# Kernel tuning notes

Hardware: AMD Instinct MI355X
Metric: run time of the kernel (lower is better)

Reference implementation:

```python
import jax, jax.numpy as jnp
import numpy as np

D_MODEL = 2048
NUM_HEADS = 16
D_K = D_MODEL // NUM_HEADS


def setup_inputs() -> dict:
    key = jax.random.key(0)
    ks = jax.random.split(key, 7)
    B, S = 4, 2048
    scale = 1.0 / np.sqrt(D_MODEL)
    return {
        "q": jax.random.normal(ks[0], (B, S, D_MODEL), dtype=jnp.float32),
        "k": jax.random.normal(ks[1], (B, S, D_MODEL), dtype=jnp.float32),
        "v": jax.random.normal(ks[2], (B, S, D_MODEL), dtype=jnp.float32),
        "w_q": jax.random.normal(ks[3], (D_MODEL, D_MODEL), dtype=jnp.float32) * scale,
        "w_k": jax.random.normal(ks[4], (D_MODEL, D_MODEL), dtype=jnp.float32) * scale,
        "w_v": jax.random.normal(ks[5], (D_MODEL, D_MODEL), dtype=jnp.float32) * scale,
        "w_o": jax.random.normal(ks[6], (D_MODEL, D_MODEL), dtype=jnp.float32) * scale,
    }


def reference(q, k, v, w_q, w_k, w_v, w_o):
    B, S, _ = q.shape
    # torch Linear (bias=False): y = x @ W.T
    def proj_heads(x, w):
        y = jnp.einsum("bsd,ed->bse", x, w)  # [B,S,D]
        return y.reshape(B, S, NUM_HEADS, D_K).transpose(0, 2, 1, 3)  # [B,H,S,Dk]

    qh = proj_heads(q, w_q)
    kh = proj_heads(k, w_k)
    vh = proj_heads(v, w_v)

    # scaled dot-product attention (padding_mask=None, dropout inactive in eval)
    logits = jnp.einsum("bhqd,bhkd->bhqk", qh, kh) / jnp.sqrt(jnp.float32(D_K))
    probs = jax.nn.softmax(logits, axis=-1)
    attn = jnp.einsum("bhqk,bhkd->bhqd", probs, vh)  # [B,H,S,Dk]

    attn = attn.transpose(0, 2, 1, 3).reshape(B, S, NUM_HEADS * D_K)
    return jnp.einsum("bsd,ed->bse", attn, w_o)
```

## Files before the change

kernel.cpp:

```cpp
#include <hip/hip_runtime.h>
#include <hip/hip_bf16.h>
#include <cstdio>

using bf16 = __hip_bfloat16;
typedef __attribute__((ext_vector_type(8))) __bf16 bf16x8;
typedef __attribute__((ext_vector_type(4))) float f32x4;

#define DI static __device__ __forceinline__

DI f32x4 mfma16(bf16x8 a, bf16x8 b, f32x4 c) {
  return __builtin_amdgcn_mfma_f32_16x16x32_bf16(a, b, c, 0, 0, 0);
}

DI void gload16(const bf16* g, bf16* lds_base) {
  __builtin_amdgcn_global_load_lds(
      (const __attribute__((address_space(1))) unsigned int*)g,
      (__attribute__((address_space(3))) unsigned int*)lds_base,
      16, 0, 0);
}

DI bf16x8 ld8(const bf16* p) { return *(const bf16x8*)p; }

DI unsigned pack_bf16(float lo, float hi) {
  bf16 l = __float2bfloat16(lo), h = __float2bfloat16(hi);
  unsigned short ul = *(unsigned short*)&l, uh = *(unsigned short*)&h;
  return ((unsigned)uh << 16) | (unsigned)ul;
}

__global__ __launch_bounds__(256) void cast_bf16_kernel(const float* __restrict__ in,
                                                        bf16* __restrict__ out, int n4) {
  int i = blockIdx.x * 256 + threadIdx.x;
  if (i >= n4) return;
  float4 v = reinterpret_cast<const float4*>(in)[i];
  bf16 o4[4] = {__float2bfloat16(v.x), __float2bfloat16(v.y),
                __float2bfloat16(v.z), __float2bfloat16(v.w)};
  reinterpret_cast<ushort4*>(out)[i] = *reinterpret_cast<ushort4*>(o4);
}

template<int OUT_F32>
__global__ __launch_bounds__(256) void gemm_bt(const bf16* __restrict__ A,
                                               const bf16* __restrict__ B,
                                               void* __restrict__ Cout,
                                               int M, int N, int K) {
  __shared__ bf16 As[128 * 64];
  __shared__ bf16 Bs[128 * 64];
  const int lane = threadIdx.x & 63;
  const int wave = threadIdx.x >> 6;
  const int wm = wave >> 1, wn = wave & 1;
  const int nwg = gridDim.x * gridDim.y;
  const int cpx = nwg >> 3;
  int id = blockIdx.x + gridDim.x * blockIdx.y;
  id = (id & 7) * cpx + (id >> 3);
  const int row0 = (id / gridDim.x) * 128;
  const int col0 = (id % gridDim.x) * 128;
  const int l4 = lane >> 4, l15 = lane & 15;
  const int lr = lane >> 3, lc = lane & 7;

  f32x4 acc[4][4] = {};

  for (int k0 = 0; k0 < K; k0 += 64) {
#pragma unroll
    for (int i = 0; i < 4; ++i) {
      const int seg = wave * 4 + i;
      const int r = seg * 8 + lr;
      const int cg = lc ^ (r & 7);
      gload16(A + (size_t)(row0 + r) * K + k0 + cg * 8, As + seg * 512);
      gload16(B + (size_t)(col0 + r) * K + k0 + cg * 8, Bs + seg * 512);
    }
    __syncthreads();
#pragma unroll
    for (int kk = 0; kk < 2; ++kk) {
      bf16x8 af[4], bfr[4];
#pragma unroll
      for (int mi = 0; mi < 4; ++mi) {
        const int r = wm * 64 + mi * 16 + l15;
        const int ch = (kk * 4 + l4) ^ (r & 7);
        af[mi] = ld8(As + r * 64 + ch * 8);
      }
#pragma unroll
      for (int ni = 0; ni < 4; ++ni) {
        const int r = wn * 64 + ni * 16 + l15;
        const int ch = (kk * 4 + l4) ^ (r & 7);
        bfr[ni] = ld8(Bs + r * 64 + ch * 8);
      }
#pragma unroll
      for (int mi = 0; mi < 4; ++mi)
#pragma unroll
        for (int ni = 0; ni < 4; ++ni)
          acc[mi][ni] = mfma16(af[mi], bfr[ni], acc[mi][ni]);
    }
    __syncthreads();
  }
#pragma unroll
  for (int mi = 0; mi < 4; ++mi)
#pragma unroll
    for (int ni = 0; ni < 4; ++ni) {
      const int r0 = row0 + wm * 64 + mi * 16 + l4 * 4;
      const int c = col0 + wn * 64 + ni * 16 + l15;
#pragma unroll
      for (int j = 0; j < 4; ++j) {
        if (OUT_F32)
          ((float*)Cout)[(size_t)(r0 + j) * N + c] = acc[mi][ni][j];
        else
          ((bf16*)Cout)[(size_t)(r0 + j) * N + c] = __float2bfloat16(acc[mi][ni][j]);
      }
    }
}

__global__ __launch_bounds__(256) void transpose_v(const bf16* __restrict__ Vp,
                                                   bf16* __restrict__ Vt) {
  constexpr int S = 2048, D = 2048, Dk = 128;
  __shared__ bf16 t[32][33];
  const int bh = blockIdx.z;
  const int b = bh >> 4, h = bh & 15;
  const int s0 = blockIdx.x * 32, d0 = blockIdx.y * 32;
  const int tx = threadIdx.x, ty = threadIdx.y;
#pragma unroll
  for (int j = 0; j < 4; ++j)
    t[ty + j * 8][tx] = Vp[(size_t)(b * S + s0 + ty + j * 8) * D + h * Dk + d0 + tx];
  __syncthreads();
#pragma unroll
  for (int j = 0; j < 4; ++j)
    Vt[(size_t)(bh * Dk + d0 + ty + j * 8) * S + s0 + tx] = t[tx][ty + j * 8];
}

__global__ __launch_bounds__(256, 2) void attn_fwd(const bf16* __restrict__ Qp,
                                                   const bf16* __restrict__ Kp,
                                                   const bf16* __restrict__ Vt,
                                                   bf16* __restrict__ ctx) {
  constexpr int S = 2048, D = 2048, Dk = 128;
  constexpr int NT = S / 64;
  constexpr float scale = 0.08838834764831845f;
  constexpr float DEFER_THR = 90.50966799187809f;
  __shared__ bf16 Ks[2][64 * 128];
  __shared__ bf16 Vs[2][128 * 64];
  __shared__ bf16 Ps[4][32 * 64];
  const int lane = threadIdx.x & 63;
  const int wave = threadIdx.x >> 6;
  int id = blockIdx.x + gridDim.x * blockIdx.y;
  id = (id & 7) * 128 + (id >> 3);
  const int bh = id >> 4, qt = id & 15;
  const int b = bh >> 4, h = bh & 15;
  const int l4 = lane >> 4, l15 = lane & 15;

  const bf16* Kbh = Kp + (size_t)b * S * D + h * Dk;
  const bf16* Vbh = Vt + (size_t)bh * Dk * S;

  auto stage = [&](int buf, int s0) {
#pragma unroll
    for (int i = 0; i < 4; ++i) {
      const int seg = wave * 4 + i;
      {
        const int r = seg * 4 + l4;
        const int cg = l15 ^ (r & 7);
        gload16(Kbh + (size_t)(s0 + r) * D + cg * 8, &Ks[buf][seg * 512]);
      }
      {
        const int d = seg * 8 + (lane >> 3);
        const int cg = (lane & 7) ^ (d & 7);
        gload16(Vbh + (size_t)d * S + s0 + cg * 8, &Vs[buf][seg * 512]);
      }
    }
  };

  bf16x8 qf[2][4];
  {
    const bf16* Qb = Qp + (size_t)(b * S + qt * 128 + wave * 32) * D + h * Dk;
#pragma unroll
    for (int mi = 0; mi < 2; ++mi)
#pragma unroll
      for (int kf = 0; kf < 4; ++kf)
        qf[mi][kf] = ld8(Qb + (size_t)(mi * 16 + l15) * D + kf * 32 + l4 * 8);
  }

  f32x4 acc[2][8] = {};
  float mrow[2] = {-1e30f, -1e30f};
  float lrow[2] = {0.f, 0.f};

  bf16* Pw = &Ps[wave][0];

  stage(0, 0);
  __syncthreads();
  int cur = 0;

  for (int t = 0; t < NT; ++t) {
    if (t + 1 < NT) stage(cur ^ 1, (t + 1) * 64);

    f32x4 sc[4][2] = {};
    __builtin_amdgcn_s_setprio(1);
#pragma unroll
    for (int kf = 0; kf < 4; ++kf) {
      bf16x8 kb[4];
#pragma unroll
      for (int ni = 0; ni < 4; ++ni) {
        const int r = ni * 16 + l15;
        const int ch = (kf * 4 + l4) ^ (r & 7);
        kb[ni] = ld8(&Ks[cur][r * 128 + ch * 8]);
      }
#pragma unroll
      for (int ni = 0; ni < 4; ++ni)
#pragma unroll
        for (int mi = 0; mi < 2; ++mi)
          sc[ni][mi] = mfma16(kb[ni], qf[mi][kf], sc[ni][mi]);
    }
    __builtin_amdgcn_s_setprio(0);

    float vm[2];
#pragma unroll
    for (int mi = 0; mi < 2; ++mi) {
      float a = fmaxf(fmaxf(sc[0][mi][0], sc[0][mi][1]), fmaxf(sc[0][mi][2], sc[0][mi][3]));
#pragma unroll
      for (int ni = 1; ni < 4; ++ni) {
        a = fmaxf(a, fmaxf(fmaxf(sc[ni][mi][0], sc[ni][mi][1]),
                           fmaxf(sc[ni][mi][2], sc[ni][mi][3])));
      }
      a = fmaxf(a, __shfl_xor(a, 16));
      a = fmaxf(a, __shfl_xor(a, 32));
      vm[mi] = a;
    }

    const int ok = (vm[0] - mrow[0] <= DEFER_THR) && (vm[1] - mrow[1] <= DEFER_THR);
    if (!__all(ok)) {
#pragma unroll
      for (int mi = 0; mi < 2; ++mi) {
        const float mnew = fmaxf(mrow[mi], vm[mi]);
        const float cr = __expf((mrow[mi] - mnew) * scale);
        mrow[mi] = mnew;
        lrow[mi] *= cr;
        float crd[4];
#pragma unroll
        for (int j = 0; j < 4; ++j) crd[j] = __shfl(cr, l4 * 4 + j);
#pragma unroll
        for (int di = 0; di < 8; ++di)
#pragma unroll
          for (int j = 0; j < 4; ++j) acc[mi][di][j] *= crd[j];
      }
    }

#pragma unroll
    for (int mi = 0; mi < 2; ++mi) {
      const float nms = -mrow[mi] * scale;
      float rs = 0.f;
      const int q_local = mi * 16 + l15;
#pragma unroll
      for (int ni = 0; ni < 4; ++ni) {
        float p0 = __expf(fmaf(sc[ni][mi][0], scale, nms));
        float p1 = __expf(fmaf(sc[ni][mi][1], scale, nms));
        float p2 = __expf(fmaf(sc[ni][mi][2], scale, nms));
        float p3 = __expf(fmaf(sc[ni][mi][3], scale, nms));
        rs += (p0 + p1) + (p2 + p3);
        uint2 w;
        w.x = pack_bf16(p0, p1);
        w.y = pack_bf16(p2, p3);
        const int c16 = (ni * 2 + (l4 >> 1)) ^ (q_local & 7);
        *reinterpret_cast<uint2*>(Pw + q_local * 64 + c16 * 8 + (l4 & 1) * 4) = w;
      }
      rs += __shfl_xor(rs, 16);
      rs += __shfl_xor(rs, 32);
      lrow[mi] += rs;
    }

    __builtin_amdgcn_s_setprio(1);
#pragma unroll
    for (int kk = 0; kk < 2; ++kk) {
      bf16x8 pa[2];
#pragma unroll
      for (int mi = 0; mi < 2; ++mi) {
        const int q_local = mi * 16 + l15;
        const int c = (kk * 4 + l4) ^ (q_local & 7);
        pa[mi] = ld8(Pw + q_local * 64 + c * 8);
      }
#pragma unroll
      for (int di = 0; di < 8; ++di) {
        const int r = di * 16 + l15;
        const int ch = (kk * 4 + l4) ^ (r & 7);
        const bf16x8 vb = ld8(&Vs[cur][r * 64 + ch * 8]);
#pragma unroll
        for (int mi = 0; mi < 2; ++mi)
          acc[mi][di] = mfma16(pa[mi], vb, acc[mi][di]);
      }
    }
    __builtin_amdgcn_s_setprio(0);
    __syncthreads();
    cur ^= 1;
  }

#pragma unroll
  for (int mi = 0; mi < 2; ++mi) {
    float invd[4];
#pragma unroll
    for (int j = 0; j < 4; ++j) invd[j] = 1.f / __shfl(lrow[mi], l4 * 4 + j);
#pragma unroll
    for (int j = 0; j < 4; ++j) {
      const size_t base =
          (size_t)(b * S + qt * 128 + wave * 32 + mi * 16 + l4 * 4 + j) * D + h * Dk + l15;
#pragma unroll
      for (int di = 0; di < 8; ++di)
        ctx[base + di * 16] = __float2bfloat16(acc[mi][di][j] * invd[j]);
    }
  }
}

extern "C" void kernel_launch(void* const* d_in, const int* in_sizes, int n_in,
                              void* d_out, int out_size, void* d_ws, size_t ws_size,
                              hipStream_t stream) {
  constexpr int B = 4, S = 2048, D = 2048, H = 16, Dk = 128;
  constexpr size_t MD = (size_t)B * S * D;
  constexpr size_t DD = (size_t)D * D;

  const float* q  = (const float*)d_in[0];
  const float* k  = (const float*)d_in[1];
  const float* v  = (const float*)d_in[2];
  const float* wq = (const float*)d_in[3];
  const float* wk = (const float*)d_in[4];
  const float* wv = (const float*)d_in[5];
  const float* wo = (const float*)d_in[6];

  bf16* ws = (bf16*)d_ws;
  bf16* xb = ws + 0 * MD;
  bf16* Vp = ws + 1 * MD;
  bf16* Vt = ws + 2 * MD;
  bf16* wb = ws + 3 * MD;
  bf16* Qp = (bf16*)d_out;
  bf16* Kp = Qp + MD;

  const size_t need = (3 * MD + DD) * sizeof(bf16);
  if (ws_size < need)
    fprintf(stderr, "kernel_launch: ws too small (%zu < %zu)\n", ws_size, need);

  auto cast = [&](const float* src, bf16* dst, size_t n) {
    const int n4 = (int)(n / 4);
    cast_bf16_kernel<<<dim3((n4 + 255) / 256), dim3(256), 0, stream>>>(src, dst, n4);
  };
  const dim3 gg(D / 128, (B * S) / 128);

  cast(q, xb, MD);
  cast(wq, wb, DD);
  gemm_bt<0><<<gg, dim3(256), 0, stream>>>(xb, wb, Qp, B * S, D, D);
  cast(k, xb, MD);
  cast(wk, wb, DD);
  gemm_bt<0><<<gg, dim3(256), 0, stream>>>(xb, wb, Kp, B * S, D, D);
  cast(v, xb, MD);
  cast(wv, wb, DD);
  gemm_bt<0><<<gg, dim3(256), 0, stream>>>(xb, wb, Vp, B * S, D, D);

  transpose_v<<<dim3(S / 32, Dk / 32, B * H), dim3(32, 8), 0, stream>>>(Vp, Vt);

  bf16* ctx = xb;
  attn_fwd<<<dim3(S / 128, B * H), dim3(256), 0, stream>>>(Qp, Kp, Vt, ctx);

  cast(wo, wb, DD);
  gemm_bt<1><<<gg, dim3(256), 0, stream>>>(ctx, wb, d_out, B * S, D, D);
}
```

Baseline: 779.1 us.

## Replace 128x128 GEMM with 256x256 double-buffered ping-pong pipelined GEMM

```diff
diff --git a/kernel.cpp b/kernel.cpp
--- a/kernel.cpp
+++ b/kernel.cpp
@@ -38,64 +38,161 @@
 }
 
 template<int OUT_F32>
-__global__ __launch_bounds__(256) void gemm_bt(const bf16* __restrict__ A,
-                                               const bf16* __restrict__ B,
-                                               void* __restrict__ Cout,
-                                               int M, int N, int K) {
-  __shared__ bf16 As[128 * 64];
-  __shared__ bf16 Bs[128 * 64];
+__global__ __launch_bounds__(512, 2) void gemm256(const bf16* __restrict__ A,
+                                                  const bf16* __restrict__ B,
+                                                  void* __restrict__ Cout,
+                                                  int M, int N, int K) {
+  __shared__ bf16 smem[2 * 2 * 2 * 8192];
   const int lane = threadIdx.x & 63;
   const int wave = threadIdx.x >> 6;
-  const int wm = wave >> 1, wn = wave & 1;
+  const int wm = wave >> 2, wn = wave & 3;
+  const int l4 = lane >> 4, l15 = lane & 15;
+  const int NT = K >> 6;
+
   const int nwg = gridDim.x * gridDim.y;
-  const int cpx = nwg >> 3;
   int id = blockIdx.x + gridDim.x * blockIdx.y;
-  id = (id & 7) * cpx + (id >> 3);
-  const int row0 = (id / gridDim.x) * 128;
-  const int col0 = (id % gridDim.x) * 128;
-  const int l4 = lane >> 4, l15 = lane & 15;
-  const int lr = lane >> 3, lc = lane & 7;
-
-  f32x4 acc[4][4] = {};
-
-  for (int k0 = 0; k0 < K; k0 += 64) {
-#pragma unroll
-    for (int i = 0; i < 4; ++i) {
-      const int seg = wave * 4 + i;
-      const int r = seg * 8 + lr;
-      const int cg = lc ^ (r & 7);
-      gload16(A + (size_t)(row0 + r) * K + k0 + cg * 8, As + seg * 512);
-      gload16(B + (size_t)(col0 + r) * K + k0 + cg * 8, Bs + seg * 512);
-    }
-    __syncthreads();
-#pragma unroll
-    for (int kk = 0; kk < 2; ++kk) {
-      bf16x8 af[4], bfr[4];
-#pragma unroll
-      for (int mi = 0; mi < 4; ++mi) {
-        const int r = wm * 64 + mi * 16 + l15;
-        const int ch = (kk * 4 + l4) ^ (r & 7);
-        af[mi] = ld8(As + r * 64 + ch * 8);
-      }
-#pragma unroll
-      for (int ni = 0; ni < 4; ++ni) {
-        const int r = wn * 64 + ni * 16 + l15;
-        const int ch = (kk * 4 + l4) ^ (r & 7);
-        bfr[ni] = ld8(Bs + r * 64 + ch * 8);
-      }
-#pragma unroll
-      for (int mi = 0; mi < 4; ++mi)
-#pragma unroll
-        for (int ni = 0; ni < 4; ++ni)
-          acc[mi][ni] = mfma16(af[mi], bfr[ni], acc[mi][ni]);
-    }
-    __syncthreads();
+  id = (id & 7) * (nwg >> 3) + (id >> 3);
+  const int row0 = (id / gridDim.x) * 256;
+  const int col0 = (id % gridDim.x) * 256;
+
+  auto slab = [&](int buf, int op, int half) -> bf16* {
+    return smem + (size_t)((((buf << 1) | op) << 1) | half) * 8192;
+  };
+
+  const int srow = wave * 8 + (lane >> 3);
+  const int cg = (lane & 7) ^ ((lane >> 3) & 7);
+
+  auto stageA = [&](int buf, int h, int t) {
+#pragma unroll
+    for (int j = 0; j < 2; ++j) {
+      const int rl = j * 64 + srow;
+      const int r = (rl & 63) + ((rl >> 6) << 7) + h * 64;
+      gload16(A + (size_t)(row0 + r) * K + t * 64 + cg * 8,
+              slab(buf, 0, h) + j * 4096 + wave * 512);
+    }
+  };
+  auto stageB = [&](int buf, int h, int t) {
+#pragma unroll
+    for (int j = 0; j < 2; ++j) {
+      const int rl = j * 64 + srow;
+      const int r = (rl & 31) + ((rl >> 5) << 6) + h * 32;
+      gload16(B + (size_t)(col0 + r) * K + t * 64 + cg * 8,
+              slab(buf, 1, h) + j * 4096 + wave * 512);
+    }
+  };
+
+  f32x4 acc[8][4] = {};
+  bf16x8 af[4][2], bfr[2][2];
+  const int xor7 = l15 & 7;
+
+  stageA(0, 0, 0); stageB(0, 0, 0); stageA(0, 1, 0); stageB(0, 1, 0);
+  if (NT > 1) { stageA(1, 0, 1); stageB(1, 0, 1); }
+  asm volatile("s_waitcnt vmcnt(4)" ::: "memory");
+  __builtin_amdgcn_s_barrier();
+
+  for (int t = 0; t < NT; ++t) {
+    const int cur = t & 1;
+    bf16* A0p = slab(cur, 0, 0);
+    bf16* A1p = slab(cur, 0, 1);
+    bf16* B0p = slab(cur, 1, 0);
+    bf16* B1p = slab(cur, 1, 1);
+
+#pragma unroll
+    for (int mq = 0; mq < 4; ++mq)
+#pragma unroll
+      for (int kk = 0; kk < 2; ++kk)
+        af[mq][kk] = ld8(A0p + (wm * 64 + mq * 16 + l15) * 64 +
+                         (((kk * 4 + l4) ^ xor7) * 8));
+#pragma unroll
+    for (int nq = 0; nq < 2; ++nq)
+#pragma unroll
+      for (int kk = 0; kk < 2; ++kk)
+        bfr[nq][kk] = ld8(B0p + (wn * 32 + nq * 16 + l15) * 64 +
+                          (((kk * 4 + l4) ^ xor7) * 8));
+    if (t + 1 < NT) stageA(cur ^ 1, 1, t + 1);
+    __builtin_amdgcn_s_barrier();
+    __builtin_amdgcn_s_setprio(1);
+#pragma unroll
+    for (int mq = 0; mq < 4; ++mq)
+#pragma unroll
+      for (int nq = 0; nq < 2; ++nq)
+#pragma unroll
+        for (int kk = 0; kk < 2; ++kk)
+          acc[mq][nq] = mfma16(af[mq][kk], bfr[nq][kk], acc[mq][nq]);
+    __builtin_amdgcn_s_setprio(0);
+    __builtin_amdgcn_s_barrier();
+
+#pragma unroll
+    for (int nq = 0; nq < 2; ++nq)
+#pragma unroll
+      for (int kk = 0; kk < 2; ++kk)
+        bfr[nq][kk] = ld8(B1p + (wn * 32 + nq * 16 + l15) * 64 +
+                          (((kk * 4 + l4) ^ xor7) * 8));
+    if (t + 1 < NT) stageB(cur ^ 1, 1, t + 1);
+    __builtin_amdgcn_s_barrier();
+    __builtin_amdgcn_s_setprio(1);
+#pragma unroll
+    for (int mq = 0; mq < 4; ++mq)
+#pragma unroll
+      for (int nq = 0; nq < 2; ++nq)
+#pragma unroll
+        for (int kk = 0; kk < 2; ++kk)
+          acc[mq][2 + nq] = mfma16(af[mq][kk], bfr[nq][kk], acc[mq][2 + nq]);
+    __builtin_amdgcn_s_setprio(0);
+    __builtin_amdgcn_s_barrier();
+
+#pragma unroll
+    for (int mq = 0; mq < 4; ++mq)
+#pragma unroll
+      for (int kk = 0; kk < 2; ++kk)
+        af[mq][kk] = ld8(A1p + (wm * 64 + mq * 16 + l15) * 64 +
+                         (((kk * 4 + l4) ^ xor7) * 8));
+#pragma unroll
+    for (int nq = 0; nq < 2; ++nq)
+#pragma unroll
+      for (int kk = 0; kk < 2; ++kk)
+        bfr[nq][kk] = ld8(B0p + (wn * 32 + nq * 16 + l15) * 64 +
+                          (((kk * 4 + l4) ^ xor7) * 8));
+    if (t + 2 < NT) stageA(cur, 0, t + 2);
+    __builtin_amdgcn_s_barrier();
+    __builtin_amdgcn_s_setprio(1);
+#pragma unroll
+    for (int mq = 0; mq < 4; ++mq)
+#pragma unroll
+      for (int nq = 0; nq < 2; ++nq)
+#pragma unroll
+        for (int kk = 0; kk < 2; ++kk)
+          acc[4 + mq][nq] = mfma16(af[mq][kk], bfr[nq][kk], acc[4 + mq][nq]);
+    __builtin_amdgcn_s_setprio(0);
+    __builtin_amdgcn_s_barrier();
+
+#pragma unroll
+    for (int nq = 0; nq < 2; ++nq)
+#pragma unroll
+      for (int kk = 0; kk < 2; ++kk)
+        bfr[nq][kk] = ld8(B1p + (wn * 32 + nq * 16 + l15) * 64 +
+                          (((kk * 4 + l4) ^ xor7) * 8));
+    if (t + 2 < NT) stageB(cur, 0, t + 2);
+    __builtin_amdgcn_s_barrier();
+    __builtin_amdgcn_s_setprio(1);
+#pragma unroll
+    for (int mq = 0; mq < 4; ++mq)
+#pragma unroll
+      for (int nq = 0; nq < 2; ++nq)
+#pragma unroll
+        for (int kk = 0; kk < 2; ++kk)
+          acc[4 + mq][2 + nq] = mfma16(af[mq][kk], bfr[nq][kk], acc[4 + mq][2 + nq]);
+    __builtin_amdgcn_s_setprio(0);
+    if (t + 2 < NT) asm volatile("s_waitcnt vmcnt(4)" ::: "memory");
+    else            asm volatile("s_waitcnt vmcnt(0)" ::: "memory");
+    __builtin_amdgcn_s_barrier();
   }
-#pragma unroll
-  for (int mi = 0; mi < 4; ++mi)
+
+#pragma unroll
+  for (int mi = 0; mi < 8; ++mi)
 #pragma unroll
     for (int ni = 0; ni < 4; ++ni) {
-      const int r0 = row0 + wm * 64 + mi * 16 + l4 * 4;
+      const int r0 = row0 + wm * 128 + mi * 16 + l4 * 4;
       const int c = col0 + wn * 64 + ni * 16 + l15;
 #pragma unroll
       for (int j = 0; j < 4; ++j) {
@@ -332,17 +429,17 @@
     const int n4 = (int)(n / 4);
     cast_bf16_kernel<<<dim3((n4 + 255) / 256), dim3(256), 0, stream>>>(src, dst, n4);
   };
-  const dim3 gg(D / 128, (B * S) / 128);
+  const dim3 gg(D / 256, (B * S) / 256);
 
   cast(q, xb, MD);
   cast(wq, wb, DD);
-  gemm_bt<0><<<gg, dim3(256), 0, stream>>>(xb, wb, Qp, B * S, D, D);
+  gemm256<0><<<gg, dim3(512), 0, stream>>>(xb, wb, Qp, B * S, D, D);
   cast(k, xb, MD);
   cast(wk, wb, DD);
-  gemm_bt<0><<<gg, dim3(256), 0, stream>>>(xb, wb, Kp, B * S, D, D);
+  gemm256<0><<<gg, dim3(512), 0, stream>>>(xb, wb, Kp, B * S, D, D);
   cast(v, xb, MD);
   cast(wv, wb, DD);
-  gemm_bt<0><<<gg, dim3(256), 0, stream>>>(xb, wb, Vp, B * S, D, D);
+  gemm256<0><<<gg, dim3(512), 0, stream>>>(xb, wb, Vp, B * S, D, D);
 
   transpose_v<<<dim3(S / 32, Dk / 32, B * H), dim3(32, 8), 0, stream>>>(Vp, Vt);
 
@@ -350,5 +447,5 @@
   attn_fwd<<<dim3(S / 128, B * H), dim3(256), 0, stream>>>(Qp, Kp, Vt, ctx);
 
   cast(wo, wb, DD);
-  gemm_bt<1><<<gg, dim3(256), 0, stream>>>(ctx, wb, d_out, B * S, D, D);
-}
+  gemm256<1><<<gg, dim3(512), 0, stream>>>(ctx, wb, d_out, B * S, D, D);
+}
```

After: 706.9 us. 1.1x faster.
